# Performance work log

Hardware: AMD Instinct MI355X
Metric: run time of the kernel (lower is better)

## Reference

```python
import jax, jax.numpy as jnp
import numpy as np

B, M, T, L, K = 64, 16, 2048, 64, 32
N = T - L + 1  # 1985 sliding-window positions


def setup_inputs() -> dict:
    key = jax.random.key(0)
    k1, k2, k3 = jax.random.split(key, 3)
    x = jax.random.normal(k1, (B, M, T), dtype=jnp.float32)
    # shapelets initialized uniform(-1, 1) as in nn.init.uniform_
    shapelets = jax.random.uniform(k2, (K, L), dtype=jnp.float32, minval=-1.0, maxval=1.0)
    # penalty maps (learned; zeros at init, random here for a non-trivial weighting)
    penalty_maps = 0.1 * jax.random.normal(k3, (K, M, N), dtype=jnp.float32)
    return {"x": x, "shapelets": shapelets, "penalty_maps": penalty_maps}


def reference(x, shapelets, penalty_maps):
    # x: (B, M, T); shapelets: (K, L); penalty_maps: (K, M, N)
    Lw = shapelets.shape[1]
    n_pos = x.shape[2] - Lw + 1
    # sliding-window view: (B, M, N, L), equivalent to torch unfold(dim=2, size=L, step=1)
    idx = jnp.arange(n_pos)[:, None] + jnp.arange(Lw)[None, :]
    sub = x[:, :, idx]  # (B, M, N, L)

    def per_shapelet(args):
        shp, pmap = args  # (L,), (M, N)
        # raw squared L2 distance over window, per channel/position: (B, M, N)
        raw = jnp.sum((sub - shp[None, None, None, :]) ** 2, axis=3)
        pen = jax.nn.elu(-pmap) + 2.0  # (M, N)
        wd = jnp.sum(raw * pen[None], axis=1)  # sum over channels -> (B, N)
        return jnp.min(wd, axis=1)  # min over positions -> (B,)

    # sequential map over the K shapelets avoids a Kx blow-up of the (B,M,N,L) intermediate
    feats = jax.lax.map(per_shapelet, (shapelets, penalty_maps))  # (K, B)
    return feats.T  # (B, K)
```

## Files before the change

kernel.cpp:

```cpp
#include <hip/hip_runtime.h>
#include <hip/hip_bf16.h>

#define B_ 64
#define M_ 16
#define T_ 2048
#define L_ 64
#define K_ 32
#define N_ (T_ - L_ + 1)
#define TN 64
#define NTH 256
#define XROW 144
#define STSTR 72

typedef __attribute__((ext_vector_type(8))) short bf16x8;
typedef __attribute__((ext_vector_type(4))) float f32x4;

__device__ __forceinline__ unsigned short f2bf(float f) {
    __hip_bfloat16 h = __float2bfloat16(f);
    return __builtin_bit_cast(unsigned short, h);
}

__device__ __forceinline__ float elu_pen(float p) {
    return (p < 0.f) ? (2.f - p) : (__expf(-p) + 1.f);
}

__global__ __launch_bounds__(NTH, 4)
void shapelet_mfma_kernel(const float* __restrict__ x,
                          const float* __restrict__ shp,
                          const float* __restrict__ pmap,
                          unsigned* __restrict__ out) {
    __shared__ __align__(16) unsigned short xbuf4[M_][4][XROW];
    __shared__ __align__(16) unsigned short st[K_][STSTR];
    __shared__ __align__(16) float sqw[M_][TN];
    __shared__ float ssb[K_];

    const int tid = threadIdx.x;
    const int n0 = blockIdx.x * TN;
    const int b  = blockIdx.y;
    const bool fast = (n0 + 2 * TN <= T_);

    for (int i = tid; i < K_ * 16; i += NTH) {
        const int k = i >> 4, l4 = (i & 15) * 4;
        float4 v = *(const float4*)(shp + k * L_ + l4);
        ushort4 sv = { f2bf(v.x), f2bf(v.y), f2bf(v.z), f2bf(v.w) };
        *(ushort4*)&st[k][l4] = sv;
    }
    if (tid < K_) {
        float s = 0.f;
        for (int l = 0; l < L_; ++l) { float v = shp[tid * L_ + l]; s = fmaf(v, v, s); }
        ssb[tid] = s;
    }

    const float* xb = x + ((size_t)b * M_) * T_ + n0;
    for (int g = tid; g < M_ * 31; g += NTH) {
        const int m = g / 31, j4 = (g - m * 31) * 4;
        const float* src = xb + m * T_ + j4;
        float h[8];
        if (fast) {
            float4 v0 = *(const float4*)src;
            float4 v1 = *(const float4*)(src + 4);
            h[0] = v0.x; h[1] = v0.y; h[2] = v0.z; h[3] = v0.w;
            h[4] = v1.x; h[5] = v1.y; h[6] = v1.z; h[7] = v1.w;
        } else {
#pragma unroll
            for (int i = 0; i < 8; ++i)
                h[i] = (n0 + j4 + i < T_) ? src[i] : 0.f;
        }
        unsigned short hb[8];
#pragma unroll
        for (int i = 0; i < 8; ++i) hb[i] = f2bf(h[i]);
#pragma unroll
        for (int s = 0; s < 4; ++s) {
            ushort4 sv = { hb[s], hb[s + 1], hb[s + 2], hb[s + 3] };
            *(ushort4*)&xbuf4[m][s][j4] = sv;
        }
    }
    if (tid < M_ * 8) {
        const int m = tid >> 3, j0 = (tid & 7) * 8;
        const float* xr = x + ((size_t)b * M_ + m) * T_ + n0;
        float s = 0.f;
        if (fast) {
#pragma unroll
            for (int qd = 0; qd < 16; ++qd) {
                float4 v = *(const float4*)(xr + j0 + qd * 4);
                s = fmaf(v.x, v.x, s); s = fmaf(v.y, v.y, s);
                s = fmaf(v.z, v.z, s); s = fmaf(v.w, v.w, s);
            }
            sqw[m][j0] = s;
#pragma unroll
            for (int d = 1; d < 8; ++d) {
                float a = xr[j0 + d + L_ - 1], r = xr[j0 + d - 1];
                s += a * a - r * r;
                sqw[m][j0 + d] = s;
            }
        } else {
            for (int l = 0; l < L_; ++l) {
                float v = (n0 + j0 + l < T_) ? xr[j0 + l] : 0.f;
                s = fmaf(v, v, s);
            }
            sqw[m][j0] = s;
            for (int d = 1; d < 8; ++d) {
                float a = (n0 + j0 + d + L_ - 1 < T_) ? xr[j0 + d + L_ - 1] : 0.f;
                float r = (n0 + j0 + d - 1 < T_) ? xr[j0 + d - 1] : 0.f;
                s += a * a - r * r;
                sqw[m][j0 + d] = s;
            }
        }
    }
    __syncthreads();

    const int lane = tid & 63;
    const int w  = tid >> 6;
    const int rl = lane & 15;
    const int q  = lane >> 4;
    const int sp = rl & 3;
    const int e0 = 16 * w + 8 * q + (rl & ~3);
    const int eq = e0 >> 2;
    const int nrow = n0 + 16 * w + 4 * q;

    bf16x8 bfr[2][2];
#pragma unroll
    for (int t = 0; t < 2; ++t)
#pragma unroll
        for (int h = 0; h < 2; ++h)
            bfr[t][h] = *(const bf16x8*)&st[16 * t + rl][8 * q + 32 * h];

    const float ssk0 = ssb[rl], ssk1 = ssb[16 + rl];

    const float* pr0 = pmap + (size_t)rl * (M_ * N_) + nrow;
    const float* pr1 = pr0 + (size_t)16 * M_ * N_;

    f32x4 wd0 = (f32x4)0.f, wd1 = (f32x4)0.f;
    const f32x4 zero = (f32x4)0.f;

    auto mstep = [&](int m, float4 pm0, float4 pm1) {
        const uint2* prow = (const uint2*)&xbuf4[m][sp][0];
        uint2 lo0 = prow[eq],     hi0 = prow[eq + 1];
        uint2 lo1 = prow[eq + 8], hi1 = prow[eq + 9];
        union { uint2 u2[2]; bf16x8 v; } fa0, fa1;
        fa0.u2[0] = lo0; fa0.u2[1] = hi0;
        fa1.u2[0] = lo1; fa1.u2[1] = hi1;

        f32x4 c0_ = __builtin_amdgcn_mfma_f32_16x16x32_bf16(fa0.v, bfr[0][0], zero, 0, 0, 0);
        c0_       = __builtin_amdgcn_mfma_f32_16x16x32_bf16(fa1.v, bfr[0][1], c0_, 0, 0, 0);
        f32x4 c1_ = __builtin_amdgcn_mfma_f32_16x16x32_bf16(fa0.v, bfr[1][0], zero, 0, 0, 0);
        c1_       = __builtin_amdgcn_mfma_f32_16x16x32_bf16(fa1.v, bfr[1][1], c1_, 0, 0, 0);

        const float pv0[4] = { pm0.x, pm0.y, pm0.z, pm0.w };
        const float pv1[4] = { pm1.x, pm1.y, pm1.z, pm1.w };
        f32x4 sq = *(const f32x4*)&sqw[m][16 * w + 4 * q];
#pragma unroll
        for (int r = 0; r < 4; ++r) {
            float pe0 = elu_pen(pv0[r]);
            float pe1 = elu_pen(pv1[r]);
            float u0 = fmaf(-2.f, c0_[r], sq[r] + ssk0);
            wd0[r] = fmaf(pe0, u0, wd0[r]);
            float u1 = fmaf(-2.f, c1_[r], sq[r] + ssk1);
            wd1[r] = fmaf(pe1, u1, wd1[r]);
        }
    };

    if (fast) {
        float4 pa0 = *(const float4*)(pr0);
        float4 pa1 = *(const float4*)(pr1);
        float4 pb0 = *(const float4*)(pr0 + N_);
        float4 pb1 = *(const float4*)(pr1 + N_);
        for (int mp = 0; mp < M_ / 2; ++mp) {
            const int m = 2 * mp;
            float4 c0 = pa0, c1 = pa1, d0 = pb0, d1 = pb1;
            if (mp + 1 < M_ / 2) {
                const float* q0 = pr0 + (size_t)(m + 2) * N_;
                const float* q1 = pr1 + (size_t)(m + 2) * N_;
                pa0 = *(const float4*)(q0);
                pa1 = *(const float4*)(q1);
                pb0 = *(const float4*)(q0 + N_);
                pb1 = *(const float4*)(q1 + N_);
            }
            mstep(m, c0, c1);
            mstep(m + 1, d0, d1);
        }
    } else {
        for (int m = 0; m < M_; ++m) {
            float4 pm0 = make_float4(0.f, 0.f, 0.f, 0.f);
            float4 pm1 = make_float4(0.f, 0.f, 0.f, 0.f);
            const float* r0_ = pr0 + (size_t)m * N_;
            const float* r1_ = pr1 + (size_t)m * N_;
            if (nrow     < N_) { pm0.x = r0_[0]; pm1.x = r1_[0]; }
            if (nrow + 1 < N_) { pm0.y = r0_[1]; pm1.y = r1_[1]; }
            if (nrow + 2 < N_) { pm0.z = r0_[2]; pm1.z = r1_[2]; }
            if (nrow + 3 < N_) { pm0.w = r0_[3]; pm1.w = r1_[3]; }
            mstep(m, pm0, pm1);
        }
    }

    __syncthreads();
    float* red = (float*)&sqw[0][0];
#pragma unroll
    for (int t = 0; t < 2; ++t) {
        float lmin = __int_as_float(0x7F800000);
        const f32x4 wdv = t ? wd1 : wd0;
#pragma unroll
        for (int r = 0; r < 4; ++r)
            if (nrow + r < N_) lmin = fminf(lmin, wdv[r]);
        lmin = fminf(lmin, __shfl_xor(lmin, 16));
        lmin = fminf(lmin, __shfl_xor(lmin, 32));
        if (q == 0) red[w * 32 + t * 16 + rl] = lmin;
    }
    __syncthreads();
    if (tid < K_) {
        float v = fminf(fminf(red[tid], red[32 + tid]),
                        fminf(red[64 + tid], red[96 + tid]));
        atomicMin(out + (size_t)b * K_ + tid, __float_as_uint(fmaxf(v, 0.f)));
    }
}

extern "C" void kernel_launch(void* const* d_in, const int* in_sizes, int n_in,
                              void* d_out, int out_size, void* d_ws, size_t ws_size,
                              hipStream_t stream) {
    const float* x    = (const float*)d_in[0];
    const float* shp  = (const float*)d_in[1];
    const float* pmap = (const float*)d_in[2];
    unsigned* out = (unsigned*)d_out;
    (void)d_ws; (void)ws_size;

    hipMemsetAsync(d_out, 0xFF, (size_t)B_ * K_ * sizeof(unsigned), stream);

    dim3 grid((N_ + TN - 1) / TN, B_);
    shapelet_mfma_kernel<<<grid, dim3(NTH), 0, stream>>>(x, shp, pmap, out);
}
```

Before: 109.2 us.

## Precompute ELU penalty into tiled workspace and split staging work across thread halves

Adds a pre-kernel that evaluates the ELU penalty once per (k,m,n), stores it in a tile-major padded layout in workspace, and also computes shapelet squared norms and initializes the output. This replaces the memsetAsync. The main kernel no longer recomputes exp per batch row and reads aligned contiguous penalty vectors, which removes the slow boundary path. It also issues the penalty prefetch before the staging phase and splits staging between two thread halves. The cost is an extra launch plus writing and re-reading a 4 MB penalty buffer.

Result: slower. 117.2 us (+7.3%).

```diff
diff --git a/kernel.cpp b/kernel.cpp
--- a/kernel.cpp
+++ b/kernel.cpp
@@ -8,9 +8,12 @@
 #define K_ 32
 #define N_ (T_ - L_ + 1)
 #define TN 64
+#define NT_ 32
 #define NTH 256
 #define XROW 144
 #define STSTR 72
+#define PENK (NT_ * M_ * 64)
+#define PENSZ (K_ * PENK)
 
 typedef __attribute__((ext_vector_type(8))) short bf16x8;
 typedef __attribute__((ext_vector_type(4))) float f32x4;
@@ -24,90 +27,56 @@
     return (p < 0.f) ? (2.f - p) : (__expf(-p) + 1.f);
 }
 
+__global__ void pen_init_kernel(const float* __restrict__ pmap,
+                                const float* __restrict__ shp,
+                                float* __restrict__ pen,
+                                float* __restrict__ ss_ws,
+                                unsigned* __restrict__ out) {
+    const int gid = blockIdx.x * 256 + threadIdx.x;
+    if (gid < B_ * K_) out[gid] = 0x7F800000u;
+    if (gid < K_) {
+        float s = 0.f;
+        for (int l = 0; l < L_; ++l) { float v = shp[gid * L_ + l]; s = fmaf(v, v, s); }
+        ss_ws[gid] = s;
+    }
+    if (gid < PENSZ / 4) {
+        const int o = gid * 4;
+        const int nin = o & 63;
+        const int m   = (o >> 6) & 15;
+        const int nt  = (o >> 10) & 31;
+        const int k   = o >> 15;
+        const int n   = nt * TN + nin;
+        const float* src = pmap + ((size_t)k * M_ + m) * N_ + n;
+        float p[4];
+        if (n + 3 < N_) {
+            float4 v = *(const float4*)src;
+            p[0] = v.x; p[1] = v.y; p[2] = v.z; p[3] = v.w;
+        } else {
+#pragma unroll
+            for (int i = 0; i < 4; ++i) p[i] = (n + i < N_) ? src[i] : 0.f;
+        }
+        float4 r;
+        r.x = elu_pen(p[0]); r.y = elu_pen(p[1]);
+        r.z = elu_pen(p[2]); r.w = elu_pen(p[3]);
+        *(float4*)(pen + o) = r;
+    }
+}
+
 __global__ __launch_bounds__(NTH, 4)
 void shapelet_mfma_kernel(const float* __restrict__ x,
                           const float* __restrict__ shp,
-                          const float* __restrict__ pmap,
+                          const float* __restrict__ pen,
+                          const float* __restrict__ ss_ws,
                           unsigned* __restrict__ out) {
     __shared__ __align__(16) unsigned short xbuf4[M_][4][XROW];
     __shared__ __align__(16) unsigned short st[K_][STSTR];
     __shared__ __align__(16) float sqw[M_][TN];
-    __shared__ float ssb[K_];
 
     const int tid = threadIdx.x;
-    const int n0 = blockIdx.x * TN;
+    const int bx = blockIdx.x;
+    const int n0 = bx * TN;
     const int b  = blockIdx.y;
     const bool fast = (n0 + 2 * TN <= T_);
-
-    for (int i = tid; i < K_ * 16; i += NTH) {
-        const int k = i >> 4, l4 = (i & 15) * 4;
-        float4 v = *(const float4*)(shp + k * L_ + l4);
-        ushort4 sv = { f2bf(v.x), f2bf(v.y), f2bf(v.z), f2bf(v.w) };
-        *(ushort4*)&st[k][l4] = sv;
-    }
-    if (tid < K_) {
-        float s = 0.f;
-        for (int l = 0; l < L_; ++l) { float v = shp[tid * L_ + l]; s = fmaf(v, v, s); }
-        ssb[tid] = s;
-    }
-
-    const float* xb = x + ((size_t)b * M_) * T_ + n0;
-    for (int g = tid; g < M_ * 31; g += NTH) {
-        const int m = g / 31, j4 = (g - m * 31) * 4;
-        const float* src = xb + m * T_ + j4;
-        float h[8];
-        if (fast) {
-            float4 v0 = *(const float4*)src;
-            float4 v1 = *(const float4*)(src + 4);
-            h[0] = v0.x; h[1] = v0.y; h[2] = v0.z; h[3] = v0.w;
-            h[4] = v1.x; h[5] = v1.y; h[6] = v1.z; h[7] = v1.w;
-        } else {
-#pragma unroll
-            for (int i = 0; i < 8; ++i)
-                h[i] = (n0 + j4 + i < T_) ? src[i] : 0.f;
-        }
-        unsigned short hb[8];
-#pragma unroll
-        for (int i = 0; i < 8; ++i) hb[i] = f2bf(h[i]);
-#pragma unroll
-        for (int s = 0; s < 4; ++s) {
-            ushort4 sv = { hb[s], hb[s + 1], hb[s + 2], hb[s + 3] };
-            *(ushort4*)&xbuf4[m][s][j4] = sv;
-        }
-    }
-    if (tid < M_ * 8) {
-        const int m = tid >> 3, j0 = (tid & 7) * 8;
-        const float* xr = x + ((size_t)b * M_ + m) * T_ + n0;
-        float s = 0.f;
-        if (fast) {
-#pragma unroll
-            for (int qd = 0; qd < 16; ++qd) {
-                float4 v = *(const float4*)(xr + j0 + qd * 4);
-                s = fmaf(v.x, v.x, s); s = fmaf(v.y, v.y, s);
-                s = fmaf(v.z, v.z, s); s = fmaf(v.w, v.w, s);
-            }
-            sqw[m][j0] = s;
-#pragma unroll
-            for (int d = 1; d < 8; ++d) {
-                float a = xr[j0 + d + L_ - 1], r = xr[j0 + d - 1];
-                s += a * a - r * r;
-                sqw[m][j0 + d] = s;
-            }
-        } else {
-            for (int l = 0; l < L_; ++l) {
-                float v = (n0 + j0 + l < T_) ? xr[j0 + l] : 0.f;
-                s = fmaf(v, v, s);
-            }
-            sqw[m][j0] = s;
-            for (int d = 1; d < 8; ++d) {
-                float a = (n0 + j0 + d + L_ - 1 < T_) ? xr[j0 + d + L_ - 1] : 0.f;
-                float r = (n0 + j0 + d - 1 < T_) ? xr[j0 + d - 1] : 0.f;
-                s += a * a - r * r;
-                sqw[m][j0 + d] = s;
-            }
-        }
-    }
-    __syncthreads();
 
     const int lane = tid & 63;
     const int w  = tid >> 6;
@@ -118,17 +87,88 @@
     const int eq = e0 >> 2;
     const int nrow = n0 + 16 * w + 4 * q;
 
+    const float ssk0 = ss_ws[rl], ssk1 = ss_ws[16 + rl];
+
+    const float* pb0 = pen + (size_t)rl * PENK + (size_t)bx * (M_ * 64) + (16 * w + 4 * q);
+    const float* pb1 = pb0 + (size_t)16 * PENK;
+
+    float4 pa0 = *(const float4*)(pb0);
+    float4 pa1 = *(const float4*)(pb1);
+    float4 pc0 = *(const float4*)(pb0 + 64);
+    float4 pc1 = *(const float4*)(pb1 + 64);
+
+    if (tid < 128) {
+        const int m = tid >> 3, j0 = (tid & 7) * 8;
+        const float* xr = x + ((size_t)b * M_ + m) * T_ + n0;
+        float s = 0.f;
+        if (fast) {
+#pragma unroll
+            for (int qd = 0; qd < 16; ++qd) {
+                float4 v = *(const float4*)(xr + j0 + qd * 4);
+                s = fmaf(v.x, v.x, s); s = fmaf(v.y, v.y, s);
+                s = fmaf(v.z, v.z, s); s = fmaf(v.w, v.w, s);
+            }
+            sqw[m][j0] = s;
+#pragma unroll
+            for (int d = 1; d < 8; ++d) {
+                float a = xr[j0 + d + L_ - 1], r = xr[j0 + d - 1];
+                s += a * a - r * r;
+                sqw[m][j0 + d] = s;
+            }
+        } else {
+            for (int l = 0; l < L_; ++l) {
+                float v = (n0 + j0 + l < T_) ? xr[j0 + l] : 0.f;
+                s = fmaf(v, v, s);
+            }
+            sqw[m][j0] = s;
+            for (int d = 1; d < 8; ++d) {
+                float a = (n0 + j0 + d + L_ - 1 < T_) ? xr[j0 + d + L_ - 1] : 0.f;
+                float r = (n0 + j0 + d - 1 < T_) ? xr[j0 + d - 1] : 0.f;
+                s += a * a - r * r;
+                sqw[m][j0 + d] = s;
+            }
+        }
+    } else {
+        const int t2 = tid - 128;
+        const float* xb = x + ((size_t)b * M_) * T_ + n0;
+        for (int g = t2; g < M_ * 31; g += 128) {
+            const int m = g / 31, j4 = (g - m * 31) * 4;
+            const float* src = xb + m * T_ + j4;
+            float h[8];
+            if (fast) {
+                float4 v0 = *(const float4*)src;
+                float4 v1 = *(const float4*)(src + 4);
+                h[0] = v0.x; h[1] = v0.y; h[2] = v0.z; h[3] = v0.w;
+                h[4] = v1.x; h[5] = v1.y; h[6] = v1.z; h[7] = v1.w;
+            } else {
+#pragma unroll
+                for (int i = 0; i < 8; ++i)
+                    h[i] = (n0 + j4 + i < T_) ? src[i] : 0.f;
+            }
+            unsigned short hb[8];
+#pragma unroll
+            for (int i = 0; i < 8; ++i) hb[i] = f2bf(h[i]);
+#pragma unroll
+            for (int s = 0; s < 4; ++s) {
+                ushort4 sv = { hb[s], hb[s + 1], hb[s + 2], hb[s + 3] };
+                *(ushort4*)&xbuf4[m][s][j4] = sv;
+            }
+        }
+        for (int i = t2; i < K_ * 16; i += 128) {
+            const int k = i >> 4, l4 = (i & 15) * 4;
+            float4 v = *(const float4*)(shp + k * L_ + l4);
+            ushort4 sv = { f2bf(v.x), f2bf(v.y), f2bf(v.z), f2bf(v.w) };
+            *(ushort4*)&st[k][l4] = sv;
+        }
+    }
+    __syncthreads();
+
     bf16x8 bfr[2][2];
 #pragma unroll
     for (int t = 0; t < 2; ++t)
 #pragma unroll
         for (int h = 0; h < 2; ++h)
             bfr[t][h] = *(const bf16x8*)&st[16 * t + rl][8 * q + 32 * h];
-
-    const float ssk0 = ssb[rl], ssk1 = ssb[16 + rl];
-
-    const float* pr0 = pmap + (size_t)rl * (M_ * N_) + nrow;
-    const float* pr1 = pr0 + (size_t)16 * M_ * N_;
 
     f32x4 wd0 = (f32x4)0.f, wd1 = (f32x4)0.f;
     const f32x4 zero = (f32x4)0.f;
@@ -146,51 +186,31 @@
         f32x4 c1_ = __builtin_amdgcn_mfma_f32_16x16x32_bf16(fa0.v, bfr[1][0], zero, 0, 0, 0);
         c1_       = __builtin_amdgcn_mfma_f32_16x16x32_bf16(fa1.v, bfr[1][1], c1_, 0, 0, 0);
 
-        const float pv0[4] = { pm0.x, pm0.y, pm0.z, pm0.w };
-        const float pv1[4] = { pm1.x, pm1.y, pm1.z, pm1.w };
+        const float pe0[4] = { pm0.x, pm0.y, pm0.z, pm0.w };
+        const float pe1[4] = { pm1.x, pm1.y, pm1.z, pm1.w };
         f32x4 sq = *(const f32x4*)&sqw[m][16 * w + 4 * q];
 #pragma unroll
         for (int r = 0; r < 4; ++r) {
-            float pe0 = elu_pen(pv0[r]);
-            float pe1 = elu_pen(pv1[r]);
             float u0 = fmaf(-2.f, c0_[r], sq[r] + ssk0);
-            wd0[r] = fmaf(pe0, u0, wd0[r]);
+            wd0[r] = fmaf(pe0[r], u0, wd0[r]);
             float u1 = fmaf(-2.f, c1_[r], sq[r] + ssk1);
-            wd1[r] = fmaf(pe1, u1, wd1[r]);
+            wd1[r] = fmaf(pe1[r], u1, wd1[r]);
         }
     };
 
-    if (fast) {
-        float4 pa0 = *(const float4*)(pr0);
-        float4 pa1 = *(const float4*)(pr1);
-        float4 pb0 = *(const float4*)(pr0 + N_);
-        float4 pb1 = *(const float4*)(pr1 + N_);
-        for (int mp = 0; mp < M_ / 2; ++mp) {
-            const int m = 2 * mp;
-            float4 c0 = pa0, c1 = pa1, d0 = pb0, d1 = pb1;
-            if (mp + 1 < M_ / 2) {
-                const float* q0 = pr0 + (size_t)(m + 2) * N_;
-                const float* q1 = pr1 + (size_t)(m + 2) * N_;
-                pa0 = *(const float4*)(q0);
-                pa1 = *(const float4*)(q1);
-                pb0 = *(const float4*)(q0 + N_);
-                pb1 = *(const float4*)(q1 + N_);
-            }
-            mstep(m, c0, c1);
-            mstep(m + 1, d0, d1);
-        }
-    } else {
-        for (int m = 0; m < M_; ++m) {
-            float4 pm0 = make_float4(0.f, 0.f, 0.f, 0.f);
-            float4 pm1 = make_float4(0.f, 0.f, 0.f, 0.f);
-            const float* r0_ = pr0 + (size_t)m * N_;
-            const float* r1_ = pr1 + (size_t)m * N_;
-            if (nrow     < N_) { pm0.x = r0_[0]; pm1.x = r1_[0]; }
-            if (nrow + 1 < N_) { pm0.y = r0_[1]; pm1.y = r1_[1]; }
-            if (nrow + 2 < N_) { pm0.z = r0_[2]; pm1.z = r1_[2]; }
-            if (nrow + 3 < N_) { pm0.w = r0_[3]; pm1.w = r1_[3]; }
-            mstep(m, pm0, pm1);
-        }
+    for (int mp = 0; mp < M_ / 2; ++mp) {
+        const int m = 2 * mp;
+        float4 c0 = pa0, c1 = pa1, d0 = pc0, d1 = pc1;
+        if (mp + 1 < M_ / 2) {
+            const float* q0 = pb0 + (size_t)(m + 2) * 64;
+            const float* q1 = pb1 + (size_t)(m + 2) * 64;
+            pa0 = *(const float4*)(q0);
+            pa1 = *(const float4*)(q1);
+            pc0 = *(const float4*)(q0 + 64);
+            pc1 = *(const float4*)(q1 + 64);
+        }
+        mstep(m, c0, c1);
+        mstep(m + 1, d0, d1);
     }
 
     __syncthreads();
@@ -221,10 +241,12 @@
     const float* shp  = (const float*)d_in[1];
     const float* pmap = (const float*)d_in[2];
     unsigned* out = (unsigned*)d_out;
-    (void)d_ws; (void)ws_size;
-
-    hipMemsetAsync(d_out, 0xFF, (size_t)B_ * K_ * sizeof(unsigned), stream);
-
-    dim3 grid((N_ + TN - 1) / TN, B_);
-    shapelet_mfma_kernel<<<grid, dim3(NTH), 0, stream>>>(x, shp, pmap, out);
-}
+    float* pen   = (float*)d_ws;
+    float* ss_ws = pen + PENSZ;
+
+    pen_init_kernel<<<dim3(PENSZ / 4 / 256), dim3(256), 0, stream>>>(
+        pmap, shp, pen, ss_ws, out);
+
+    dim3 grid(NT_, B_);
+    shapelet_mfma_kernel<<<grid, dim3(NTH), 0, stream>>>(x, shp, pen, ss_ws, out);
+}
```
